# Optimization experiments

Hardware: AMD Instinct MI355X
Metric: run time of the kernel (lower is better)

Reference implementation:

```python
import jax, jax.numpy as jnp
import numpy as np

B, S, K, D, H, COND, MR = 4, 1024, 1024, 1024, 16, 1024, 4
HD = D // H  # 64
INV_SQRT_HD = 1.0 / float(np.sqrt(HD))
GELU_C = 0.7978845608028654  # sqrt(2/pi)


def _make_rope(seqlen):
    pos = jnp.arange(seqlen, dtype=jnp.float32)
    inv = 1.0 / (10000.0 ** (jnp.arange(0, HD // 2, dtype=jnp.float32) * 2.0 / HD))
    ang = pos[:, None] * inv[None, :]                     # [S, HD/2]
    cos = jnp.concatenate([jnp.cos(ang), jnp.cos(ang)], -1)  # [S, HD]
    sin = jnp.concatenate([jnp.sin(ang), jnp.sin(ang)], -1)
    return cos[None, :, None, :], sin[None, :, None, :]   # [1,S,1,HD]


def setup_inputs():
    key = jax.random.key(0)
    ks = jax.random.split(key, 14)
    rn = lambda k, shape, s=0.02: jax.random.normal(k, shape, jnp.float32) * s
    cos_q, sin_q = _make_rope(S)
    cos_k, sin_k = _make_rope(K)
    ada_b = jnp.zeros((6 * D,), jnp.float32)
    ada_b = ada_b.at[2 * D:3 * D].set(0.5).at[5 * D:6 * D].set(0.5)  # gate_msa, gate_mlp init
    return {
        "q_x": jax.random.normal(ks[0], (B, S, D), jnp.float32),
        "kv_x": jax.random.normal(ks[1], (B, K, D), jnp.float32),
        "t_cond": jax.random.normal(ks[2], (B, COND), jnp.float32),
        "cos_q": cos_q, "sin_q": sin_q, "cos_k": cos_k, "sin_k": sin_k,
        "group_idxs": jax.random.randint(ks[3], (B, S), 0, 4, jnp.int32),
        "query_enabled": jax.random.randint(ks[4], (B, S), 0, 2, jnp.int32).astype(bool),
        "qn_w": jnp.ones((D,), jnp.float32),
        "kvn_w": jnp.ones((D,), jnp.float32),
        "n2_w": jnp.ones((D,), jnp.float32),
        "Wq": rn(ks[5], (D, D)), "Wkv": rn(ks[6], (D, 2 * D)), "Wo": rn(ks[7], (D, D)),
        "W1": rn(ks[8], (D, MR * D)), "b1": jnp.zeros((MR * D,), jnp.float32),
        "W2": rn(ks[9], (MR * D, D)), "b2": jnp.zeros((D,), jnp.float32),
        "adaW": rn(ks[10], (COND, 6 * D)), "adab": ada_b,
    }


def layer_norm(x, w):
    mu = jnp.mean(x, -1, keepdims=True)
    var = jnp.var(x, -1, keepdims=True)
    return (x - mu) * jax.lax.rsqrt(var + 1e-5) * w


def rope(x, cos, sin):
    # x: [B,S,H,HD]; cos/sin: [1,S,1,HD]; rotate_half convention
    x1, x2 = jnp.split(x, 2, axis=-1)
    return x * cos + jnp.concatenate([-x2, x1], -1) * sin


def gelu_tanh(x):
    return 0.5 * x * (1.0 + jnp.tanh(GELU_C * (x + 0.044715 * x * x * x)))


def reference(q_x, kv_x, t_cond, cos_q, sin_q, cos_k, sin_k, group_idxs, query_enabled,
              qn_w, kvn_w, n2_w, Wq, Wkv, Wo, W1, b1, W2, b2, adaW, adab):
    # adaLN modulation (inference: dropout disabled -> bias_dropout_add_scale = scale*x + residual)
    mod = (t_cond @ adaW + adab)[:, None, :]               # [B,1,6D]
    sh_msa, sc_msa, g_msa, sh_mlp, sc_mlp, g_mlp = jnp.split(mod, 6, axis=-1)

    qn = layer_norm(q_x, qn_w)
    kvn = layer_norm(kv_x, kvn_w)
    qn = qn * (1.0 + sc_msa) + sh_msa                      # modulate_fused

    q = (qn @ Wq).reshape(B, S, H, HD)
    kv = (kvn @ Wkv).reshape(B, K, 2, H, HD)
    k, v = kv[:, :, 0], kv[:, :, 1]
    q = rope(q, cos_q, sin_q)
    k = rope(k, cos_k, sin_k)

    # group cross-attn mask: attend only where groups differ
    attend = group_idxs[:, :, None] != group_idxs[:, None, :]  # [B,S,K]
    scores = jnp.einsum('bqhd,bkhd->bhqk', q, k) * INV_SQRT_HD
    scores = jnp.where(attend[:, None, :, :], scores, -1e9)
    p = jax.nn.softmax(scores, axis=-1)
    attn = jnp.einsum('bhqk,bkhd->bqhd', p, v).reshape(B, S, D)

    x = g_msa * (attn @ Wo) + q_x                          # fused bias-dropout-add-scale (inference)
    gate = query_enabled[..., None].astype(x.dtype)
    x = x * gate + q_x * (1.0 - gate)                      # gated_update

    x_mid = x
    h = layer_norm(x, n2_w) * (1.0 + sc_mlp) + sh_mlp
    h = gelu_tanh(h @ W1 + b1) @ W2 + b2
    x = g_mlp * h + x_mid
    x = x * gate + x_mid * (1.0 - gate)
    return x
```

## Files before the change

### kernel.cpp

```cpp
#include <hip/hip_runtime.h>
#include <hip/hip_bf16.h>
#include <math.h>

typedef __bf16 bf16_t;
typedef __attribute__((ext_vector_type(8))) __bf16 bf16x8;
typedef __attribute__((ext_vector_type(4))) __bf16 bf16x4;
typedef __attribute__((ext_vector_type(4))) float f32x4;

__global__ __launch_bounds__(256) void compact_kernel(
    const int* __restrict__ qen, int* __restrict__ idx, int* __restrict__ McPtr)
{
  __shared__ int cnts[256];
  int t = threadIdx.x;
  int flags[16], c = 0;
#pragma unroll
  for (int i = 0; i < 16; ++i) {
    flags[i] = qen[t * 16 + i] != 0;
    c += flags[i];
  }
  cnts[t] = c;
  __syncthreads();
  for (int off = 1; off < 256; off <<= 1) {
    int v = cnts[t];
    if (t >= off) v += cnts[t - off];
    __syncthreads();
    cnts[t] = v;
    __syncthreads();
  }
  int p = cnts[t] - c;
  int total = cnts[255];
#pragma unroll
  for (int i = 0; i < 16; ++i)
    if (flags[i]) idx[p++] = t * 16 + i;
  if (t == 0) *McPtr = total;
  for (int j = total + t; j < 4096; j += 256) idx[j] = 0;
}

__global__ __launch_bounds__(256) void copy_disabled_kernel(
    const int* __restrict__ qen, const float* __restrict__ qx,
    float* __restrict__ out)
{
  int row = blockIdx.x;
  if (qen[row]) return;
  int tid = threadIdx.x;
  ((float4*)(out + (size_t)row * 1024))[tid] =
      ((const float4*)(qx + (size_t)row * 1024))[tid];
}

__global__ __launch_bounds__(256) void mod_init_kernel(
    const float* __restrict__ adab, float* __restrict__ mod)
{
  int i = blockIdx.x * 256 + threadIdx.x;
  mod[i] = adab[i % 6144];
}

__global__ __launch_bounds__(256) void mod_partial_kernel(
    const float* __restrict__ tc, const float* __restrict__ adaW,
    float* __restrict__ mod)
{
  __shared__ float st[4][128];
  int tid = threadIdx.x, z = blockIdx.y;
  for (int i = tid; i < 512; i += 256)
    st[i >> 7][i & 127] = tc[(i >> 7) * 1024 + z * 128 + (i & 127)];
  __syncthreads();
  int col = blockIdx.x * 256 + tid;
  float a0 = 0.f, a1 = 0.f, a2 = 0.f, a3 = 0.f;
  for (int k = 0; k < 128; ++k) {
    float wv = adaW[(size_t)(z * 128 + k) * 6144 + col];
    a0 = fmaf(st[0][k], wv, a0);
    a1 = fmaf(st[1][k], wv, a1);
    a2 = fmaf(st[2][k], wv, a2);
    a3 = fmaf(st[3][k], wv, a3);
  }
  atomicAdd(&mod[col], a0);
  atomicAdd(&mod[6144 + col], a1);
  atomicAdd(&mod[2 * 6144 + col], a2);
  atomicAdd(&mod[3 * 6144 + col], a3);
}

__global__ __launch_bounds__(256) void transpose_all(
    const float* __restrict__ Wq, const float* __restrict__ Wkv,
    const float* __restrict__ Wo, const float* __restrict__ W1,
    const float* __restrict__ W2,
    bf16_t* __restrict__ oWq, bf16_t* __restrict__ oWkv,
    bf16_t* __restrict__ oWo, bf16_t* __restrict__ oW1,
    bf16_t* __restrict__ oW2)
{
  __shared__ float tile[32][33];
  int bid = blockIdx.x;
  const float* in; bf16_t* out; int R, C, gx, local;
  if (bid < 1024)      { in = Wq;  out = oWq;  R = 1024; C = 1024; gx = 32;  local = bid; }
  else if (bid < 3072) { in = Wkv; out = oWkv; R = 1024; C = 2048; gx = 64;  local = bid - 1024; }
  else if (bid < 4096) { in = Wo;  out = oWo;  R = 1024; C = 1024; gx = 32;  local = bid - 3072; }
  else if (bid < 8192) { in = W1;  out = oW1;  R = 1024; C = 4096; gx = 128; local = bid - 4096; }
  else                 { in = W2;  out = oW2;  R = 4096; C = 1024; gx = 32;  local = bid - 8192; }
  int c0 = (local % gx) * 32, r0 = (local / gx) * 32;
  int tx = threadIdx.x, ty = threadIdx.y;
#pragma unroll
  for (int i = 0; i < 4; ++i)
    tile[ty + i * 8][tx] = in[(size_t)(r0 + ty + i * 8) * C + c0 + tx];
  __syncthreads();
#pragma unroll
  for (int i = 0; i < 4; ++i)
    out[(size_t)(c0 + ty + i * 8) * R + r0 + tx] = (bf16_t)tile[tx][ty + i * 8];
}

__global__ __launch_bounds__(256) void ln_both_kernel(
    const float* __restrict__ qx, const float* __restrict__ kvx,
    const float* __restrict__ qnw, const float* __restrict__ kvnw,
    const float* __restrict__ mod,
    bf16_t* __restrict__ qn_out, bf16_t* __restrict__ kvn_out)
{
  int rowg = blockIdx.x;
  bool isQ = rowg < 4096;
  int row = isQ ? rowg : rowg - 4096;
  int b = row >> 10;
  int tid = threadIdx.x;
  const float* x = (isQ ? qx : kvx) + (size_t)row * 1024;
  const float* wgt = isQ ? qnw : kvnw;
  bf16_t* outp = (isQ ? qn_out : kvn_out) + (size_t)row * 1024;

  float4 v = ((const float4*)x)[tid];
  float s = v.x + v.y + v.z + v.w;
  float s2 = v.x * v.x + v.y * v.y + v.z * v.z + v.w * v.w;
#pragma unroll
  for (int off = 32; off > 0; off >>= 1) {
    s += __shfl_down(s, off, 64);
    s2 += __shfl_down(s2, off, 64);
  }
  __shared__ float ps[4], ps2[4];
  if ((tid & 63) == 0) { ps[tid >> 6] = s; ps2[tid >> 6] = s2; }
  __syncthreads();
  float mu = (ps[0] + ps[1] + ps[2] + ps[3]) * (1.0f / 1024.0f);
  float var = (ps2[0] + ps2[1] + ps2[2] + ps2[3]) * (1.0f / 1024.0f) - mu * mu;
  float rs = rsqrtf(var + 1e-5f);
  float xv[4] = {v.x, v.y, v.z, v.w};
#pragma unroll
  for (int i = 0; i < 4; ++i) {
    int col = tid * 4 + i;
    float n = (xv[i] - mu) * rs * wgt[col];
    if (isQ)
      n = n * (1.0f + mod[b * 6144 + 1024 + col]) + mod[b * 6144 + col];
    outp[col] = (bf16_t)n;
  }
}

__global__ __launch_bounds__(256) void reduce_q_rope_kernel(
    const bf16_t* __restrict__ P0, const bf16_t* __restrict__ P1,
    const float* __restrict__ cosq, const float* __restrict__ sinq,
    bf16_t* __restrict__ qr)
{
  int t = blockIdx.x * 256 + threadIdx.x;
  int hd = t & 31;
  int h = (t >> 5) & 15;
  int s = (t >> 9) & 1023;
  int b = t >> 19;
  size_t base = ((size_t)(b * 1024 + s)) * 1024 + h * 64 + hd;
  float v1 = (float)P0[base] + (float)P1[base];
  float v2 = (float)P0[base + 32] + (float)P1[base + 32];
  float c1 = cosq[s * 64 + hd], s1 = sinq[s * 64 + hd];
  float c2 = cosq[s * 64 + hd + 32], s2 = sinq[s * 64 + hd + 32];
  float o1 = (v1 * c1 - v2 * s1) * 0.125f;
  float o2 = (v2 * c2 + v1 * s2) * 0.125f;
  size_t ob = ((size_t)(b * 16 + h) * 1024 + s) * 64 + hd;
  qr[ob] = (bf16_t)o1;
  qr[ob + 32] = (bf16_t)o2;
}

__global__ __launch_bounds__(256) void reduce_kv_kernel(
    const bf16_t* __restrict__ P0, const bf16_t* __restrict__ P1,
    const float* __restrict__ cosk, const float* __restrict__ sink,
    bf16_t* __restrict__ kr, bf16_t* __restrict__ vt)
{
  __shared__ float ks[64][65];
  __shared__ float vs[64][65];
  int bh = blockIdx.x;
  int b = bh >> 4, h = bh & 15;
  int n0 = blockIdx.y * 64;
  int tid = threadIdx.x;
#pragma unroll
  for (int it = 0; it < 16; ++it) {
    int linear = tid + it * 256;
    int nl = linear >> 6, hd = linear & 63;
    size_t gi = ((size_t)(b * 1024 + n0 + nl)) * 2048 + h * 64 + hd;
    ks[nl][hd] = (float)P0[gi] + (float)P1[gi];
    vs[hd][nl] = (float)P0[gi + 1024] + (float)P1[gi + 1024];
  }
  __syncthreads();
#pragma unroll
  for (int it = 0; it < 16; ++it) {
    int linear = tid + it * 256;
    int nl = linear >> 6, hd = linear & 63;
    float kv = ks[nl][hd];
    float pv = ks[nl][hd ^ 32];
    float c = cosk[(n0 + nl) * 64 + hd], sn = sink[(n0 + nl) * 64 + hd];
    float o = (hd < 32) ? (kv * c - pv * sn) : (kv * c + pv * sn);
    kr[((size_t)bh * 1024 + n0 + nl) * 64 + hd] = (bf16_t)o;
    vt[((size_t)bh * 64 + nl) * 1024 + n0 + hd] = (bf16_t)vs[nl][hd];
  }
}

__global__ __launch_bounds__(256, 2) void attn_kernel(
    const bf16_t* __restrict__ qr, const bf16_t* __restrict__ kr,
    const bf16_t* __restrict__ vt, const int* __restrict__ grp,
    bf16_t* __restrict__ outp)
{
  __shared__ bf16_t Ks[64 * 72];
  __shared__ bf16_t Vs[64 * 72];
  __shared__ bf16_t Ps[128 * 72];
  __shared__ int gk[64];
  const int bh = blockIdx.x;
  const int b = bh >> 4, h = bh & 15;
  const int qBase = blockIdx.y * 128;
  const int tid = threadIdx.x, lane = tid & 63, w = tid >> 6;
  const int l15 = lane & 15, l4 = lane >> 4;
  const f32x4 zero = {0.f, 0.f, 0.f, 0.f};

  bf16x8 qA0[2], qA1[2];
  int gqr[2][4];
#pragma unroll
  for (int s = 0; s < 2; ++s) {
    int row = qBase + w * 32 + s * 16;
    const bf16_t* qp = qr + ((size_t)bh * 1024 + row + l15) * 64;
    qA0[s] = *(const bf16x8*)(qp + l4 * 8);
    qA1[s] = *(const bf16x8*)(qp + 32 + l4 * 8);
#pragma unroll
    for (int r = 0; r < 4; ++r) gqr[s][r] = grp[b * 1024 + row + l4 * 4 + r];
  }

  f32x4 oacc[2][4];
  float rsum[2][4];
#pragma unroll
  for (int s = 0; s < 2; ++s)
#pragma unroll
    for (int i = 0; i < 4; ++i) { oacc[s][i] = zero; rsum[s][i] = 0.f; }

  for (int kt = 0; kt < 16; ++kt) {
    __syncthreads();
#pragma unroll
    for (int i = 0; i < 2; ++i) {
      int c = tid * 2 + i;
      int r = c >> 3, cc = (c & 7) * 8;
      *(bf16x8*)(Ks + r * 72 + cc) =
          *(const bf16x8*)(kr + ((size_t)bh * 1024 + kt * 64 + r) * 64 + cc);
      *(bf16x8*)(Vs + r * 72 + cc) =
          *(const bf16x8*)(vt + ((size_t)bh * 64 + r) * 1024 + kt * 64 + cc);
    }
    if (tid < 64) gk[tid] = grp[b * 1024 + kt * 64 + tid];
    __syncthreads();

    int gkv[4];
    bf16x8 kf0[4], kf1[4];
#pragma unroll
    for (int nt = 0; nt < 4; ++nt) {
      gkv[nt] = gk[nt * 16 + l15];
      kf0[nt] = *(const bf16x8*)(Ks + (nt * 16 + l15) * 72 + l4 * 8);
      kf1[nt] = *(const bf16x8*)(Ks + (nt * 16 + l15) * 72 + 32 + l4 * 8);
    }

#pragma unroll
    for (int s = 0; s < 2; ++s) {
      f32x4 sacc[4];
#pragma unroll
      for (int nt = 0; nt < 4; ++nt) sacc[nt] = zero;
#pragma unroll
      for (int nt = 0; nt < 4; ++nt) {
        sacc[nt] = __builtin_amdgcn_mfma_f32_16x16x32_bf16(qA0[s], kf0[nt], sacc[nt], 0, 0, 0);
        sacc[nt] = __builtin_amdgcn_mfma_f32_16x16x32_bf16(qA1[s], kf1[nt], sacc[nt], 0, 0, 0);
      }
#pragma unroll
      for (int r = 0; r < 4; ++r) {
        int gq = gqr[s][r];
        float acc = 0.f;
#pragma unroll
        for (int nt = 0; nt < 4; ++nt) {
          float sv = sacc[nt][r] + ((gq == gkv[nt]) ? -60.f : 0.f);
          float p = __expf(sv);
          acc += p;
          Ps[(w * 32 + s * 16 + l4 * 4 + r) * 72 + nt * 16 + l15] = (bf16_t)p;
        }
        rsum[s][r] += acc;
      }
    }
#pragma unroll
    for (int s = 0; s < 2; ++s) {
      const bf16_t* pp = Ps + (w * 32 + s * 16 + l15) * 72;
      bf16x8 pf0 = *(const bf16x8*)(pp + l4 * 8);
      bf16x8 pf1 = *(const bf16x8*)(pp + 32 + l4 * 8);
#pragma unroll
      for (int nt = 0; nt < 4; ++nt) {
        bf16x8 vf0 = *(const bf16x8*)(Vs + (nt * 16 + l15) * 72 + l4 * 8);
        bf16x8 vf1 = *(const bf16x8*)(Vs + (nt * 16 + l15) * 72 + 32 + l4 * 8);
        oacc[s][nt] = __builtin_amdgcn_mfma_f32_16x16x32_bf16(pf0, vf0, oacc[s][nt], 0, 0, 0);
        oacc[s][nt] = __builtin_amdgcn_mfma_f32_16x16x32_bf16(pf1, vf1, oacc[s][nt], 0, 0, 0);
      }
    }
  }

#pragma unroll
  for (int s = 0; s < 2; ++s)
#pragma unroll
    for (int r = 0; r < 4; ++r) {
      float t = rsum[s][r];
      t += __shfl_xor(t, 1, 64);
      t += __shfl_xor(t, 2, 64);
      t += __shfl_xor(t, 4, 64);
      t += __shfl_xor(t, 8, 64);
      rsum[s][r] = 1.f / t;
    }
#pragma unroll
  for (int s = 0; s < 2; ++s)
#pragma unroll
    for (int r = 0; r < 4; ++r) {
      int srow = qBase + w * 32 + s * 16 + l4 * 4 + r;
      float inv = rsum[s][r];
#pragma unroll
      for (int nt = 0; nt < 4; ++nt)
        outp[((size_t)(b * 1024 + srow)) * 1024 + h * 64 + nt * 16 + l15] =
            (bf16_t)(oacc[s][nt][r] * inv);
    }
}

__device__ __forceinline__ void stage16(const bf16_t* gp, bf16_t* lp) {
  __builtin_amdgcn_global_load_lds(
      (__attribute__((address_space(1))) void*)gp,
      (__attribute__((address_space(3))) void*)lp, 16, 0, 0);
}

__global__ __launch_bounds__(256, 2) void gemm_bt_full(
    const bf16_t* __restrict__ A, const bf16_t* __restrict__ Bt,
    int M, int N, int Kd, int kChunk, bf16_t* __restrict__ Cb)
{
  __shared__ bf16_t sA[128 * 64];
  __shared__ bf16_t sB[128 * 64];
  const int tid = threadIdx.x;
  const int lane = tid & 63, w = tid >> 6;
  const int wr = w >> 1, wc = w & 1;

  const int gx = gridDim.x, gy = gridDim.y;
  const int L = blockIdx.y * gx + blockIdx.x;
  const int xcd = L & 7, id2 = L >> 3;
  const int ry = gy >> 2, rx = gx >> 1;
  const int tileY = (xcd & 3) * ry + (id2 % ry);
  const int tileX = (xcd >> 2) * rx + (id2 / ry);
  const int rowBase = tileY * 128;
  const int colBase = tileX * 128;

  const int l15 = lane & 15, l4 = lane >> 4;
  const int srow = lane >> 3;
  const int sg = lane & 7;
  const int scol = (sg ^ srow) * 8;
  const int rl = l15 & 7;
  const int g0 = (l4 ^ rl) * 8;
  const int g1 = ((4 + l4) ^ rl) * 8;

  const f32x4 zero = {0.f, 0.f, 0.f, 0.f};
  f32x4 acc[4][4];
#pragma unroll
  for (int i = 0; i < 4; ++i)
#pragma unroll
    for (int j = 0; j < 4; ++j) acc[i][j] = zero;

  const bf16_t* aBase = A + (size_t)(rowBase + w * 32 + srow) * Kd + scol;
  const bf16_t* bBase = Bt + (size_t)(colBase + w * 32 + srow) * Kd + scol;

  const int kStart = blockIdx.z * kChunk;
  for (int k0 = kStart; k0 < kStart + kChunk; k0 += 64) {
    __syncthreads();
#pragma unroll
    for (int i = 0; i < 4; ++i) {
      stage16(aBase + (size_t)i * 8 * Kd + k0, sA + (w * 32 + i * 8) * 64);
      stage16(bBase + (size_t)i * 8 * Kd + k0, sB + (w * 32 + i * 8) * 64);
    }
    __syncthreads();
    bf16x8 af[4], bfr[4];
#pragma unroll
    for (int mt = 0; mt < 4; ++mt)
      af[mt] = *(const bf16x8*)(sA + (wr * 64 + mt * 16 + l15) * 64 + g0);
#pragma unroll
    for (int nt = 0; nt < 4; ++nt)
      bfr[nt] = *(const bf16x8*)(sB + (wc * 64 + nt * 16 + l15) * 64 + g0);
#pragma unroll
    for (int mt = 0; mt < 4; ++mt)
#pragma unroll
      for (int nt = 0; nt < 4; ++nt)
        acc[mt][nt] = __builtin_amdgcn_mfma_f32_16x16x32_bf16(af[mt], bfr[nt],
                                                              acc[mt][nt], 0, 0, 0);
#pragma unroll
    for (int mt = 0; mt < 4; ++mt)
      af[mt] = *(const bf16x8*)(sA + (wr * 64 + mt * 16 + l15) * 64 + g1);
#pragma unroll
    for (int nt = 0; nt < 4; ++nt)
      bfr[nt] = *(const bf16x8*)(sB + (wc * 64 + nt * 16 + l15) * 64 + g1);
#pragma unroll
    for (int mt = 0; mt < 4; ++mt)
#pragma unroll
      for (int nt = 0; nt < 4; ++nt)
        acc[mt][nt] = __builtin_amdgcn_mfma_f32_16x16x32_bf16(af[mt], bfr[nt],
                                                              acc[mt][nt], 0, 0, 0);
  }

  const size_t zOff = (size_t)blockIdx.z * M * N;
#pragma unroll
  for (int mt = 0; mt < 4; ++mt)
#pragma unroll
    for (int nt = 0; nt < 4; ++nt) {
      int col = colBase + wc * 64 + nt * 16 + l15;
#pragma unroll
      for (int r = 0; r < 4; ++r) {
        int rr = rowBase + wr * 64 + mt * 16 + l4 * 4 + r;
        Cb[zOff + (size_t)rr * N + col] = (bf16_t)acc[mt][nt][r];
      }
    }
}

template <int EPI, int GATHER>
__global__ __launch_bounds__(256, 2) void gemm64_c(
    const bf16_t* __restrict__ A, const bf16_t* __restrict__ Bt,
    int N, int Kd, int kChunk, bf16_t* __restrict__ Cb,
    const float* __restrict__ bias,
    const int* __restrict__ idxG, const int* __restrict__ McPtr)
{
  __shared__ bf16_t sA[64 * 64];
  __shared__ bf16_t sB[128 * 64];
  const int Mc = *McPtr;
  const int gx = gridDim.x;
  const int L = blockIdx.y * gx + blockIdx.x;
  const int xcd = L & 7, id2 = L >> 3;
  const int tileY = (id2 / gx) * 8 + xcd;
  const int tileX = id2 % gx;
  const int rowBase = tileY * 64;
  if (rowBase >= Mc) return;
  const int colBase = tileX * 128;

  const int tid = threadIdx.x;
  const int lane = tid & 63, w = tid >> 6;
  const int wr = w >> 1, wc = w & 1;
  const int l15 = lane & 15, l4 = lane >> 4;
  const int srow = lane >> 3;
  const int sg = lane & 7;
  const int scol = (sg ^ srow) * 8;
  const int rl = l15 & 7;
  const int g0 = (l4 ^ rl) * 8;
  const int g1 = ((4 + l4) ^ rl) * 8;

  const f32x4 zero = {0.f, 0.f, 0.f, 0.f};
  f32x4 acc[2][4];
#pragma unroll
  for (int i = 0; i < 2; ++i)
#pragma unroll
    for (int j = 0; j < 4; ++j) acc[i][j] = zero;

  const bf16_t* aB[2];
#pragma unroll
  for (int i = 0; i < 2; ++i) {
    int rowc = rowBase + w * 16 + i * 8 + srow;
    int arow = GATHER ? idxG[rowc] : rowc;
    aB[i] = A + (size_t)arow * Kd + scol;
  }
  const bf16_t* bBase = Bt + (size_t)(colBase + w * 32 + srow) * Kd + scol;

  const int kStart = blockIdx.z * kChunk;
  for (int k0 = kStart; k0 < kStart + kChunk; k0 += 64) {
    __syncthreads();
#pragma unroll
    for (int i = 0; i < 2; ++i)
      stage16(aB[i] + k0, sA + (w * 16 + i * 8) * 64);
#pragma unroll
    for (int i = 0; i < 4; ++i)
      stage16(bBase + (size_t)i * 8 * Kd + k0, sB + (w * 32 + i * 8) * 64);
    __syncthreads();
    bf16x8 af[2], bfr[4];
#pragma unroll
    for (int mt = 0; mt < 2; ++mt)
      af[mt] = *(const bf16x8*)(sA + (wr * 32 + mt * 16 + l15) * 64 + g0);
#pragma unroll
    for (int nt = 0; nt < 4; ++nt)
      bfr[nt] = *(const bf16x8*)(sB + (wc * 64 + nt * 16 + l15) * 64 + g0);
#pragma unroll
    for (int mt = 0; mt < 2; ++mt)
#pragma unroll
      for (int nt = 0; nt < 4; ++nt)
        acc[mt][nt] = __builtin_amdgcn_mfma_f32_16x16x32_bf16(af[mt], bfr[nt],
                                                              acc[mt][nt], 0, 0, 0);
#pragma unroll
    for (int mt = 0; mt < 2; ++mt)
      af[mt] = *(const bf16x8*)(sA + (wr * 32 + mt * 16 + l15) * 64 + g1);
#pragma unroll
    for (int nt = 0; nt < 4; ++nt)
      bfr[nt] = *(const bf16x8*)(sB + (wc * 64 + nt * 16 + l15) * 64 + g1);
#pragma unroll
    for (int mt = 0; mt < 2; ++mt)
#pragma unroll
      for (int nt = 0; nt < 4; ++nt)
        acc[mt][nt] = __builtin_amdgcn_mfma_f32_16x16x32_bf16(af[mt], bfr[nt],
                                                              acc[mt][nt], 0, 0, 0);
  }

  const size_t zOff = (size_t)blockIdx.z * 4096 * N;
#pragma unroll
  for (int mt = 0; mt < 2; ++mt)
#pragma unroll
    for (int nt = 0; nt < 4; ++nt) {
      int col = colBase + wc * 64 + nt * 16 + l15;
#pragma unroll
      for (int r = 0; r < 4; ++r) {
        int rr = rowBase + wr * 32 + mt * 16 + l4 * 4 + r;
        float v = acc[mt][nt][r];
        if constexpr (EPI == 1) {
          float t = v + bias[col];
          float z = 0.7978845608028654f * (t + 0.044715f * t * t * t);
          float e = __expf(2.f * z);
          float g = 0.5f * t * (2.f - 2.f / (e + 1.f));
          Cb[(size_t)rr * N + col] = (bf16_t)g;
        } else {
          Cb[zOff + (size_t)rr * N + col] = (bf16_t)v;
        }
      }
    }
}

__global__ __launch_bounds__(256) void ln2_fused_kernel(
    const bf16_t* __restrict__ P, const float* __restrict__ qx,
    const float* __restrict__ n2w, const float* __restrict__ mod,
    const int* __restrict__ idxG, const int* __restrict__ McPtr,
    float* __restrict__ xbufc, bf16_t* __restrict__ xnc)
{
  int rowc = blockIdx.x;
  if (rowc >= *McPtr) return;
  int rr = idxG[rowc];
  int b = rr >> 10;
  int tid = threadIdx.x;
  size_t rc = (size_t)rowc * 1024 + tid * 4;
  bf16x4 p0 = *(const bf16x4*)(P + rc);
  bf16x4 p1 = *(const bf16x4*)(P + 4194304 + rc);
  bf16x4 p2 = *(const bf16x4*)(P + 2 * 4194304 + rc);
  bf16x4 p3 = *(const bf16x4*)(P + 3 * 4194304 + rc);
  float4 res = ((const float4*)(qx + (size_t)rr * 1024))[tid];
  float4 g = ((const float4*)(mod + b * 6144 + 2048))[tid];
  float4 x;
  x.x = fmaf(g.x, (float)p0[0] + (float)p1[0] + (float)p2[0] + (float)p3[0], res.x);
  x.y = fmaf(g.y, (float)p0[1] + (float)p1[1] + (float)p2[1] + (float)p3[1], res.y);
  x.z = fmaf(g.z, (float)p0[2] + (float)p1[2] + (float)p2[2] + (float)p3[2], res.z);
  x.w = fmaf(g.w, (float)p0[3] + (float)p1[3] + (float)p2[3] + (float)p3[3], res.w);
  *(float4*)(xbufc + rc) = x;

  float s = x.x + x.y + x.z + x.w;
  float s2 = x.x * x.x + x.y * x.y + x.z * x.z + x.w * x.w;
#pragma unroll
  for (int off = 32; off > 0; off >>= 1) {
    s += __shfl_down(s, off, 64);
    s2 += __shfl_down(s2, off, 64);
  }
  __shared__ float ps[4], ps2[4];
  if ((tid & 63) == 0) { ps[tid >> 6] = s; ps2[tid >> 6] = s2; }
  __syncthreads();
  float mu = (ps[0] + ps[1] + ps[2] + ps[3]) * (1.0f / 1024.0f);
  float var = (ps2[0] + ps2[1] + ps2[2] + ps2[3]) * (1.0f / 1024.0f) - mu * mu;
  float rs = rsqrtf(var + 1e-5f);
  float4 sc = ((const float4*)(mod + b * 6144 + 4096))[tid];
  float4 sh = ((const float4*)(mod + b * 6144 + 3072))[tid];
  float4 wv = ((const float4*)n2w)[tid];
  float xv[4] = {x.x, x.y, x.z, x.w};
  float scv[4] = {sc.x, sc.y, sc.z, sc.w};
  float shv[4] = {sh.x, sh.y, sh.z, sh.w};
  float wvv[4] = {wv.x, wv.y, wv.z, wv.w};
#pragma unroll
  for (int i = 0; i < 4; ++i) {
    float n = (xv[i] - mu) * rs * wvv[i];
    n = n * (1.0f + scv[i]) + shv[i];
    xnc[(size_t)rowc * 1024 + tid * 4 + i] = (bf16_t)n;
  }
}

__global__ __launch_bounds__(256) void final_reduce_kernel(
    const bf16_t* __restrict__ P, const float* __restrict__ b2,
    const float* __restrict__ mod, const int* __restrict__ idxG,
    const int* __restrict__ McPtr, const float* __restrict__ xbufc,
    float* __restrict__ out)
{
  int rowc = blockIdx.x;
  if (rowc >= *McPtr) return;
  int rr = idxG[rowc];
  int b = rr >> 10;
  int tid = threadIdx.x;
  size_t rc = (size_t)rowc * 1024 + tid * 4;
  bf16x4 p0 = *(const bf16x4*)(P + rc);
  bf16x4 p1 = *(const bf16x4*)(P + 4194304 + rc);
  bf16x4 p2 = *(const bf16x4*)(P + 2 * 4194304 + rc);
  bf16x4 p3 = *(const bf16x4*)(P + 3 * 4194304 + rc);
  float4 bb = ((const float4*)b2)[tid];
  float4 xm = *(const float4*)(xbufc + rc);
  float4 g = ((const float4*)(mod + b * 6144 + 5120))[tid];
  float v0 = (float)p0[0] + (float)p1[0] + (float)p2[0] + (float)p3[0] + bb.x;
  float v1 = (float)p0[1] + (float)p1[1] + (float)p2[1] + (float)p3[1] + bb.y;
  float v2 = (float)p0[2] + (float)p1[2] + (float)p2[2] + (float)p3[2] + bb.z;
  float v3 = (float)p0[3] + (float)p1[3] + (float)p2[3] + (float)p3[3] + bb.w;
  float4 o;
  o.x = fmaf(g.x, v0, xm.x);
  o.y = fmaf(g.y, v1, xm.y);
  o.z = fmaf(g.z, v2, xm.z);
  o.w = fmaf(g.w, v3, xm.w);
  *(float4*)(out + (size_t)rr * 1024 + tid * 4) = o;
}

extern "C" void kernel_launch(void* const* d_in, const int* in_sizes, int n_in,
                              void* d_out, int out_size, void* d_ws, size_t ws_size,
                              hipStream_t stream)
{
  const float* q_x    = (const float*)d_in[0];
  const float* kv_x   = (const float*)d_in[1];
  const float* t_cond = (const float*)d_in[2];
  const float* cos_q  = (const float*)d_in[3];
  const float* sin_q  = (const float*)d_in[4];
  const float* cos_k  = (const float*)d_in[5];
  const float* sin_k  = (const float*)d_in[6];
  const int*   grp    = (const int*)d_in[7];
  const int*   qen    = (const int*)d_in[8];
  const float* qn_w   = (const float*)d_in[9];
  const float* kvn_w  = (const float*)d_in[10];
  const float* n2_w   = (const float*)d_in[11];
  const float* Wq     = (const float*)d_in[12];
  const float* Wkv    = (const float*)d_in[13];
  const float* Wo     = (const float*)d_in[14];
  const float* W1     = (const float*)d_in[15];
  const float* b1     = (const float*)d_in[16];
  const float* W2     = (const float*)d_in[17];
  const float* b2     = (const float*)d_in[18];
  const float* adaW   = (const float*)d_in[19];
  const float* adab   = (const float*)d_in[20];
  float* out = (float*)d_out;

  char* ws = (char*)d_ws;
  const size_t MB = 1ull << 20;
  float*  mod    = (float*)(ws + 0);
  int*    idxL   = (int*)(ws + 98304);
  int*    McPtr  = (int*)(ws + 98304 + 16384);
  char*   wbase  = ws + 131072;
  bf16_t* Wq_t   = (bf16_t*)(wbase);
  bf16_t* Wkv_t  = (bf16_t*)(wbase + 2 * MB);
  bf16_t* Wo_t   = (bf16_t*)(wbase + 6 * MB);
  bf16_t* W1_t   = (bf16_t*)(wbase + 8 * MB);
  bf16_t* W2_t   = (bf16_t*)(wbase + 16 * MB);
  bf16_t* qn_mod = (bf16_t*)(wbase + 24 * MB);
  bf16_t* kvn    = (bf16_t*)(wbase + 32 * MB);
  bf16_t* q_r    = (bf16_t*)(wbase + 40 * MB);
  bf16_t* k_r    = (bf16_t*)(wbase + 48 * MB);
  bf16_t* v_t    = (bf16_t*)(wbase + 56 * MB);
  bf16_t* h1     = (bf16_t*)(wbase + 64 * MB);
  bf16_t* scr    = (bf16_t*)(wbase + 96 * MB);
  bf16_t* xn_c   = qn_mod;
  bf16_t* attn_o = kvn;
  float*  xbuf_c = (float*)q_r;

  compact_kernel<<<1, 256, 0, stream>>>(qen, idxL, McPtr);
  copy_disabled_kernel<<<4096, 256, 0, stream>>>(qen, q_x, out);
  mod_init_kernel<<<96, 256, 0, stream>>>(adab, mod);
  mod_partial_kernel<<<dim3(24, 8), 256, 0, stream>>>(t_cond, adaW, mod);
  transpose_all<<<12288, dim3(32, 8), 0, stream>>>(Wq, Wkv, Wo, W1, W2,
                                                   Wq_t, Wkv_t, Wo_t, W1_t, W2_t);
  ln_both_kernel<<<8192, 256, 0, stream>>>(q_x, kv_x, qn_w, kvn_w, mod,
                                           qn_mod, kvn);
  gemm_bt_full<<<dim3(8, 32, 2), 256, 0, stream>>>(qn_mod, Wq_t, 4096, 1024, 1024,
                                                   512, scr);
  reduce_q_rope_kernel<<<8192, 256, 0, stream>>>(scr, scr + 4194304, cos_q, sin_q, q_r);
  gemm_bt_full<<<dim3(16, 32, 2), 256, 0, stream>>>(kvn, Wkv_t, 4096, 2048, 1024,
                                                    512, scr);
  reduce_kv_kernel<<<dim3(64, 16), 256, 0, stream>>>(scr, scr + 8388608, cos_k, sin_k,
                                                     k_r, v_t);
  attn_kernel<<<dim3(64, 8), 256, 0, stream>>>(q_r, k_r, v_t, grp, attn_o);
  gemm64_c<4, 1><<<dim3(8, 64, 4), 256, 0, stream>>>(attn_o, Wo_t, 1024, 1024, 256,
                                                     scr, nullptr, idxL, McPtr);
  ln2_fused_kernel<<<4096, 256, 0, stream>>>(scr, q_x, n2_w, mod, idxL, McPtr,
                                             xbuf_c, xn_c);
  gemm64_c<1, 0><<<dim3(32, 64, 1), 256, 0, stream>>>(xn_c, W1_t, 4096, 1024, 1024,
                                                      h1, b1, idxL, McPtr);
  gemm64_c<4, 0><<<dim3(8, 64, 4), 256, 0, stream>>>(h1, W2_t, 1024, 4096, 1024,
                                                     scr, nullptr, idxL, McPtr);
  final_reduce_kernel<<<4096, 256, 0, stream>>>(scr, b2, mod, idxL, McPtr, xbuf_c, out);
}
```

Before: 402.0 us.

## Split attention over key halves and merge Q and KV projection GEMMs

The attention kernel now splits the key range into two halves across blockIdx.z. Each half writes unnormalized partial outputs and row sums, and a new reduce kernel adds the halves and normalizes them. This doubles the block count from 512 to 1024 to fill the GPU, and the kernel adds a fixed -60 instead of a running max, so the two halves can be added directly. The Q and KV projection GEMMs are fused into one launch of 1536 blocks to cut a launch and fill the machine. The LDS row padding drops from 72 to 68, and occupancy is raised to 4 blocks per CU. In exchange, partial outputs go through a bf16 round trip in global memory and an extra kernel runs.

Result: no change. 405.6 us (+0.9%).

```diff
diff --git a/kernel.cpp b/kernel.cpp
--- a/kernel.cpp
+++ b/kernel.cpp
@@ -200,18 +200,19 @@
   }
 }
 
-__global__ __launch_bounds__(256, 2) void attn_kernel(
+__global__ __launch_bounds__(256, 4) void attn_kernel(
     const bf16_t* __restrict__ qr, const bf16_t* __restrict__ kr,
     const bf16_t* __restrict__ vt, const int* __restrict__ grp,
-    bf16_t* __restrict__ outp)
-{
-  __shared__ bf16_t Ks[64 * 72];
-  __shared__ bf16_t Vs[64 * 72];
-  __shared__ bf16_t Ps[128 * 72];
+    bf16_t* __restrict__ Op, float* __restrict__ lbuf)
+{
+  __shared__ bf16_t Ks[64 * 68];
+  __shared__ bf16_t Vs[64 * 68];
+  __shared__ bf16_t Ps[128 * 68];
   __shared__ int gk[64];
   const int bh = blockIdx.x;
   const int b = bh >> 4, h = bh & 15;
   const int qBase = blockIdx.y * 128;
+  const int z = blockIdx.z;
   const int tid = threadIdx.x, lane = tid & 63, w = tid >> 6;
   const int l15 = lane & 15, l4 = lane >> 4;
   const f32x4 zero = {0.f, 0.f, 0.f, 0.f};
@@ -235,15 +236,15 @@
 #pragma unroll
     for (int i = 0; i < 4; ++i) { oacc[s][i] = zero; rsum[s][i] = 0.f; }
 
-  for (int kt = 0; kt < 16; ++kt) {
+  for (int kt = z * 8; kt < z * 8 + 8; ++kt) {
     __syncthreads();
 #pragma unroll
     for (int i = 0; i < 2; ++i) {
       int c = tid * 2 + i;
       int r = c >> 3, cc = (c & 7) * 8;
-      *(bf16x8*)(Ks + r * 72 + cc) =
+      *(bf16x8*)(Ks + r * 68 + cc) =
           *(const bf16x8*)(kr + ((size_t)bh * 1024 + kt * 64 + r) * 64 + cc);
-      *(bf16x8*)(Vs + r * 72 + cc) =
+      *(bf16x8*)(Vs + r * 68 + cc) =
           *(const bf16x8*)(vt + ((size_t)bh * 64 + r) * 1024 + kt * 64 + cc);
     }
     if (tid < 64) gk[tid] = grp[b * 1024 + kt * 64 + tid];
@@ -254,8 +255,8 @@
 #pragma unroll
     for (int nt = 0; nt < 4; ++nt) {
       gkv[nt] = gk[nt * 16 + l15];
-      kf0[nt] = *(const bf16x8*)(Ks + (nt * 16 + l15) * 72 + l4 * 8);
-      kf1[nt] = *(const bf16x8*)(Ks + (nt * 16 + l15) * 72 + 32 + l4 * 8);
+      kf0[nt] = *(const bf16x8*)(Ks + (nt * 16 + l15) * 68 + l4 * 8);
+      kf1[nt] = *(const bf16x8*)(Ks + (nt * 16 + l15) * 68 + 32 + l4 * 8);
     }
 
 #pragma unroll
@@ -277,20 +278,20 @@
           float sv = sacc[nt][r] + ((gq == gkv[nt]) ? -60.f : 0.f);
           float p = __expf(sv);
           acc += p;
-          Ps[(w * 32 + s * 16 + l4 * 4 + r) * 72 + nt * 16 + l15] = (bf16_t)p;
+          Ps[(w * 32 + s * 16 + l4 * 4 + r) * 68 + nt * 16 + l15] = (bf16_t)p;
         }
         rsum[s][r] += acc;
       }
     }
 #pragma unroll
     for (int s = 0; s < 2; ++s) {
-      const bf16_t* pp = Ps + (w * 32 + s * 16 + l15) * 72;
+      const bf16_t* pp = Ps + (w * 32 + s * 16 + l15) * 68;
       bf16x8 pf0 = *(const bf16x8*)(pp + l4 * 8);
       bf16x8 pf1 = *(const bf16x8*)(pp + 32 + l4 * 8);
 #pragma unroll
       for (int nt = 0; nt < 4; ++nt) {
-        bf16x8 vf0 = *(const bf16x8*)(Vs + (nt * 16 + l15) * 72 + l4 * 8);
-        bf16x8 vf1 = *(const bf16x8*)(Vs + (nt * 16 + l15) * 72 + 32 + l4 * 8);
+        bf16x8 vf0 = *(const bf16x8*)(Vs + (nt * 16 + l15) * 68 + l4 * 8);
+        bf16x8 vf1 = *(const bf16x8*)(Vs + (nt * 16 + l15) * 68 + 32 + l4 * 8);
         oacc[s][nt] = __builtin_amdgcn_mfma_f32_16x16x32_bf16(pf0, vf0, oacc[s][nt], 0, 0, 0);
         oacc[s][nt] = __builtin_amdgcn_mfma_f32_16x16x32_bf16(pf1, vf1, oacc[s][nt], 0, 0, 0);
       }
@@ -306,19 +307,34 @@
       t += __shfl_xor(t, 2, 64);
       t += __shfl_xor(t, 4, 64);
       t += __shfl_xor(t, 8, 64);
-      rsum[s][r] = 1.f / t;
+      int row = qBase + w * 32 + s * 16 + l4 * 4 + r;
+      if (l15 == 0) lbuf[z * 65536 + bh * 1024 + row] = t;
+#pragma unroll
+      for (int nt = 0; nt < 4; ++nt)
+        Op[(size_t)z * 4194304 + ((size_t)(b * 1024 + row)) * 1024 + h * 64 +
+           nt * 16 + l15] = (bf16_t)oacc[s][nt][r];
     }
-#pragma unroll
-  for (int s = 0; s < 2; ++s)
-#pragma unroll
-    for (int r = 0; r < 4; ++r) {
-      int srow = qBase + w * 32 + s * 16 + l4 * 4 + r;
-      float inv = rsum[s][r];
-#pragma unroll
-      for (int nt = 0; nt < 4; ++nt)
-        outp[((size_t)(b * 1024 + srow)) * 1024 + h * 64 + nt * 16 + l15] =
-            (bf16_t)(oacc[s][nt][r] * inv);
-    }
+}
+
+__global__ __launch_bounds__(256) void attn_reduce_kernel(
+    const bf16_t* __restrict__ Op, const float* __restrict__ lbuf,
+    bf16_t* __restrict__ attn_o)
+{
+  int row = blockIdx.x;
+  int b = row >> 10, s = row & 1023;
+  int tid = threadIdx.x;
+  int h = tid >> 4;
+  float l0 = lbuf[(b * 16 + h) * 1024 + s];
+  float l1 = lbuf[65536 + (b * 16 + h) * 1024 + s];
+  float inv = 1.f / (l0 + l1);
+  size_t ro = (size_t)row * 1024 + tid * 4;
+  bf16x4 o0 = *(const bf16x4*)(Op + ro);
+  bf16x4 o1 = *(const bf16x4*)(Op + 4194304 + ro);
+  bf16x4 o;
+#pragma unroll
+  for (int i = 0; i < 4; ++i)
+    o[i] = (bf16_t)(((float)o0[i] + (float)o1[i]) * inv);
+  *(bf16x4*)(attn_o + ro) = o;
 }
 
 __device__ __forceinline__ void stage16(const bf16_t* gp, bf16_t* lp) {
@@ -327,24 +343,36 @@
       (__attribute__((address_space(3))) void*)lp, 16, 0, 0);
 }
 
-__global__ __launch_bounds__(256, 2) void gemm_bt_full(
-    const bf16_t* __restrict__ A, const bf16_t* __restrict__ Bt,
-    int M, int N, int Kd, int kChunk, bf16_t* __restrict__ Cb)
+__global__ __launch_bounds__(256, 2) void gemm_qkv(
+    const bf16_t* __restrict__ qn, const bf16_t* __restrict__ WqT,
+    const bf16_t* __restrict__ kvn, const bf16_t* __restrict__ WkvT,
+    bf16_t* __restrict__ scr)
 {
   __shared__ bf16_t sA[128 * 64];
   __shared__ bf16_t sB[128 * 64];
   const int tid = threadIdx.x;
   const int lane = tid & 63, w = tid >> 6;
   const int wr = w >> 1, wc = w & 1;
-
-  const int gx = gridDim.x, gy = gridDim.y;
-  const int L = blockIdx.y * gx + blockIdx.x;
+  const int z = blockIdx.z;
+
+  const int L = blockIdx.y * 24 + blockIdx.x;
   const int xcd = L & 7, id2 = L >> 3;
-  const int ry = gy >> 2, rx = gx >> 1;
-  const int tileY = (xcd & 3) * ry + (id2 % ry);
-  const int tileX = (xcd >> 2) * rx + (id2 / ry);
+  const int tileY = (xcd & 3) * 8 + (id2 % 8);
+  const int tileX = (xcd >> 2) * 12 + (id2 / 8);
   const int rowBase = tileY * 128;
-  const int colBase = tileX * 128;
+
+  const bf16_t* A;
+  const bf16_t* Bt;
+  bf16_t* Cb;
+  int N, colBase;
+  size_t zOff;
+  if (tileX < 8) {
+    A = qn; Bt = WqT; N = 1024; colBase = tileX * 128;
+    Cb = scr; zOff = (size_t)z * 4194304;
+  } else {
+    A = kvn; Bt = WkvT; N = 2048; colBase = (tileX - 8) * 128;
+    Cb = scr + 8388608; zOff = (size_t)z * 8388608;
+  }
 
   const int l15 = lane & 15, l4 = lane >> 4;
   const int srow = lane >> 3;
@@ -361,16 +389,16 @@
 #pragma unroll
     for (int j = 0; j < 4; ++j) acc[i][j] = zero;
 
-  const bf16_t* aBase = A + (size_t)(rowBase + w * 32 + srow) * Kd + scol;
-  const bf16_t* bBase = Bt + (size_t)(colBase + w * 32 + srow) * Kd + scol;
-
-  const int kStart = blockIdx.z * kChunk;
-  for (int k0 = kStart; k0 < kStart + kChunk; k0 += 64) {
+  const bf16_t* aBase = A + (size_t)(rowBase + w * 32 + srow) * 1024 + scol;
+  const bf16_t* bBase = Bt + (size_t)(colBase + w * 32 + srow) * 1024 + scol;
+
+  const int kStart = z * 512;
+  for (int k0 = kStart; k0 < kStart + 512; k0 += 64) {
     __syncthreads();
 #pragma unroll
     for (int i = 0; i < 4; ++i) {
-      stage16(aBase + (size_t)i * 8 * Kd + k0, sA + (w * 32 + i * 8) * 64);
-      stage16(bBase + (size_t)i * 8 * Kd + k0, sB + (w * 32 + i * 8) * 64);
+      stage16(aBase + (size_t)i * 8 * 1024 + k0, sA + (w * 32 + i * 8) * 64);
+      stage16(bBase + (size_t)i * 8 * 1024 + k0, sB + (w * 32 + i * 8) * 64);
     }
     __syncthreads();
     bf16x8 af[4], bfr[4];
@@ -400,7 +428,6 @@
                                                               acc[mt][nt], 0, 0, 0);
   }
 
-  const size_t zOff = (size_t)blockIdx.z * M * N;
 #pragma unroll
   for (int mt = 0; mt < 4; ++mt)
 #pragma unroll
@@ -509,8 +536,8 @@
         float v = acc[mt][nt][r];
         if constexpr (EPI == 1) {
           float t = v + bias[col];
-          float z = 0.7978845608028654f * (t + 0.044715f * t * t * t);
-          float e = __expf(2.f * z);
+          float zz = 0.7978845608028654f * (t + 0.044715f * t * t * t);
+          float e = __expf(2.f * zz);
           float g = 0.5f * t * (2.f - 2.f / (e + 1.f));
           Cb[(size_t)rr * N + col] = (bf16_t)g;
         } else {
@@ -652,6 +679,8 @@
   bf16_t* xn_c   = qn_mod;
   bf16_t* attn_o = kvn;
   float*  xbuf_c = (float*)q_r;
+  bf16_t* attn_p = scr;
+  float*  lbuf   = (float*)(scr + 8388608);
 
   compact_kernel<<<1, 256, 0, stream>>>(qen, idxL, McPtr);
   copy_disabled_kernel<<<4096, 256, 0, stream>>>(qen, q_x, out);
@@ -661,14 +690,12 @@
                                                    Wq_t, Wkv_t, Wo_t, W1_t, W2_t);
   ln_both_kernel<<<8192, 256, 0, stream>>>(q_x, kv_x, qn_w, kvn_w, mod,
                                            qn_mod, kvn);
-  gemm_bt_full<<<dim3(8, 32, 2), 256, 0, stream>>>(qn_mod, Wq_t, 4096, 1024, 1024,
-                                                   512, scr);
+  gemm_qkv<<<dim3(24, 32, 2), 256, 0, stream>>>(qn_mod, Wq_t, kvn, Wkv_t, scr);
   reduce_q_rope_kernel<<<8192, 256, 0, stream>>>(scr, scr + 4194304, cos_q, sin_q, q_r);
-  gemm_bt_full<<<dim3(16, 32, 2), 256, 0, stream>>>(kvn, Wkv_t, 4096, 2048, 1024,
-                                                    512, scr);
-  reduce_kv_kernel<<<dim3(64, 16), 256, 0, stream>>>(scr, scr + 8388608, cos_k, sin_k,
-                                                     k_r, v_t);
-  attn_kernel<<<dim3(64, 8), 256, 0, stream>>>(q_r, k_r, v_t, grp, attn_o);
+  reduce_kv_kernel<<<dim3(64, 16), 256, 0, stream>>>(scr + 8388608, scr + 16777216,
+                                                     cos_k, sin_k, k_r, v_t);
+  attn_kernel<<<dim3(64, 8, 2), 256, 0, stream>>>(q_r, k_r, v_t, grp, attn_p, lbuf);
+  attn_reduce_kernel<<<4096, 256, 0, stream>>>(attn_p, lbuf, attn_o);
   gemm64_c<4, 1><<<dim3(8, 64, 4), 256, 0, stream>>>(attn_o, Wo_t, 1024, 1024, 256,
                                                      scr, nullptr, idxL, McPtr);
   ln2_fused_kernel<<<4096, 256, 0, stream>>>(scr, q_x, n2_w, mod, idxL, McPtr,
```
